# Optimization experiments

Hardware: AMD Instinct MI355X
Metric: run time of the kernel (lower is better)

## Reference

```python
import jax, jax.numpy as jnp
import numpy as np

N = 50000
E = 800000
NFEAT, NHID, NCLASS = 128, 64, 16


def _spmm(row, col, w, x):
    # out[i] = sum_{e: row[e]==i} w[e] * x[col[e]]  -- sparse adj @ x
    return jax.ops.segment_sum(x[col] * w[:, None], row, num_segments=N)


def _gcn_layer(x, row, col, w, W, b):
    return _spmm(row, col, w, x @ W) + b


def setup_inputs() -> dict:
    key = jax.random.key(0)
    ks = jax.random.split(key, 16)
    glorot = lambda k, fi, fo: jax.random.uniform(k, (fi, fo), jnp.float32, -1.0, 1.0) / jnp.sqrt(fi)
    inp = {
        "x": jax.random.normal(ks[0], (N, NFEAT), jnp.float32),
        "edge_row": jax.random.randint(ks[1], (E,), 0, N, jnp.int32),
        "edge_col": jax.random.randint(ks[2], (E,), 0, N, jnp.int32),
        "edge_weight": jax.random.uniform(ks[3], (E,), jnp.float32),
        "W1": glorot(ks[4], NFEAT, NHID), "b1": jnp.zeros((NHID,), jnp.float32),
        "W2": glorot(ks[5], NHID, NHID), "b2": jnp.zeros((NHID,), jnp.float32),
        "W3": glorot(ks[6], NHID, NHID), "b3": jnp.zeros((NHID,), jnp.float32),
        "W4": glorot(ks[7], NHID, NHID), "b4": jnp.zeros((NHID,), jnp.float32),
        "W5": glorot(ks[8], NHID, NCLASS), "b5": jnp.zeros((NCLASS,), jnp.float32),
    }
    return inp


def reference(x, edge_row, edge_col, edge_weight, W1, b1, W2, b2, W3, b3, W4, b4, W5, b5):
    # Inference mode: dropout is identity.
    e1 = _gcn_layer(x, edge_row, edge_col, edge_weight, W1, b1)
    h = jax.nn.relu(e1)
    e2 = _gcn_layer(h, edge_row, edge_col, edge_weight, W2, b2)
    h = jax.nn.relu(e2)
    e3 = _gcn_layer(h, edge_row, edge_col, edge_weight, W3, b3)
    h = jax.nn.relu(e3)
    e4 = _gcn_layer(h, edge_row, edge_col, edge_weight, W4, b4)
    h = jax.nn.relu(e4)
    e5 = _gcn_layer(h, edge_row, edge_col, edge_weight, W5, b5)
    return (jax.nn.log_softmax(e5, axis=1), e1, e2, e3, e4, e5)
```

## Files before the change

kernel.cpp:

```cpp
#include <hip/hip_runtime.h>
#include <math.h>

#define NN 50000
#define NE 800000
#define NFEAT 128
#define NHID 64
#define NCLASS 16
#define NB_SCAN ((NN + 255) / 256)
#define GB ((NN + 63) / 64)
#define SGRP 4
#define ROWS_PER_SGRP ((NN + SGRP - 1) / SGRP)
#define SCHUNKS 392
#define EMAX 1024

__device__ inline unsigned short f2bf(float f) {
    unsigned u = __builtin_bit_cast(unsigned, f);
    u += 0x7fffu + ((u >> 16) & 1u);
    return (unsigned short)(u >> 16);
}
__device__ inline float bf2f(unsigned short h) {
    return __builtin_bit_cast(float, (unsigned)h << 16);
}
__device__ inline float pk_w(unsigned v) { return bf2f((unsigned short)(v >> 16)); }
__device__ inline int pk_c(unsigned v) { return (int)(v & 0xffffu); }


__global__ __launch_bounds__(256) void hist_pack_kernel(const int* __restrict__ erow,
                                                        const int* __restrict__ ecol,
                                                        const float* __restrict__ ew,
                                                        int* __restrict__ deg,
                                                        uint2* __restrict__ rr8, int E) {
    int e = blockIdx.x * 256 + threadIdx.x;
    if (e < E) {
        int r = erow[e];
        int k = atomicAdd(&deg[r], 1);
        uint2 v;
        v.x = ((unsigned)r << 16) | (unsigned)k;
        v.y = ((unsigned)f2bf(ew[e]) << 16) | (unsigned)ecol[e];
        rr8[e] = v;
    }
}

__global__ __launch_bounds__(256) void scan_sum_kernel(const int* __restrict__ deg,
                                                       int* __restrict__ blocksum, int n) {
    __shared__ int s[256];
    const int t = threadIdx.x;
    int i = blockIdx.x * 256 + t;
    s[t] = (i < n) ? deg[i] : 0;
    __syncthreads();
#pragma unroll
    for (int off = 128; off > 0; off >>= 1) {
        if (t < off) s[t] += s[t + off];
        __syncthreads();
    }
    if (t == 0) blocksum[blockIdx.x] = s[0];
}

__global__ __launch_bounds__(256) void scan_final_kernel(const int* __restrict__ deg,
                                                         const int* __restrict__ blocksum,
                                                         int* __restrict__ row_ptr, int n) {
    __shared__ int bs[256];
    __shared__ int s[256];
    const int t = threadIdx.x;
    bs[t] = (t < NB_SCAN) ? blocksum[t] : 0;
    __syncthreads();
    for (int off = 1; off < 256; off <<= 1) {
        int u = (t >= off) ? bs[t - off] : 0;
        __syncthreads();
        bs[t] += u;
        __syncthreads();
    }
    const int blockpre = (blockIdx.x == 0) ? 0 : bs[blockIdx.x - 1];

    int i = blockIdx.x * 256 + t;
    int d = (i < n) ? deg[i] : 0;
    s[t] = d;
    __syncthreads();
    for (int off = 1; off < 256; off <<= 1) {
        int u = (t >= off) ? s[t - off] : 0;
        __syncthreads();
        s[t] += u;
        __syncthreads();
    }
    int excl = blockpre + s[t] - d;
    if (i < n) {
        row_ptr[i] = excl;
        if (i == n - 1) row_ptr[n] = excl + d;
    }
}

__global__ __launch_bounds__(256) void scatter_rank8_kernel(const uint2* __restrict__ rr8,
                                                            const int* __restrict__ row_ptr,
                                                            unsigned* __restrict__ pk, int E) {
    const int g = blockIdx.x & (SGRP - 1);
    const int chunk = blockIdx.x / SGRP;
    const int CH = (E + SCHUNKS - 1) / SCHUNKS;
    const int lo = chunk * CH;
    const int hi = (lo + CH < E) ? lo + CH : E;
    const int rlo = g * ROWS_PER_SGRP;
    const int rhi = (rlo + ROWS_PER_SGRP < NN) ? rlo + ROWS_PER_SGRP : NN;
    for (int e = lo + threadIdx.x; e < hi; e += 256) {
        uint2 v = rr8[e];
        int r = (int)(v.x >> 16);
        if (r >= rlo && r < rhi) {
            pk[row_ptr[r] + (int)(v.x & 0xffffu)] = v.y;
        }
    }
}

template <int K, bool RELU_IN>
__global__ __launch_bounds__(256) void gemm64_kernel(const float* __restrict__ in,
                                                     const float* __restrict__ Wg,
                                                     unsigned short* __restrict__ outb, int M) {
    constexpr int KC = 64;
    __shared__ float xs[KC][68];
    __shared__ float Ws[KC][64];
    const int t = threadIdx.x;
    const int tx = t % 16;
    const int ty = t / 16;
    const int r0 = blockIdx.x * 64;

    float acc[4][4];
#pragma unroll
    for (int i = 0; i < 4; i++)
#pragma unroll
        for (int j = 0; j < 4; j++) acc[i][j] = 0.f;

    for (int k0 = 0; k0 < K; k0 += KC) {
        for (int i = t * 4; i < KC * 64; i += 1024) {
            *(float4*)&Ws[i / 64][i % 64] = *(const float4*)&Wg[(size_t)k0 * 64 + i];
        }
        {
            const int r = t / 4;
            const int q = t % 4;
            const int gr = r0 + r;
#pragma unroll
            for (int i = 0; i < 4; i++) {
                int k = q * 16 + i * 4;
                float4 v;
                if (gr < M)
                    v = *(const float4*)&in[(size_t)gr * K + k0 + k];
                else
                    v = make_float4(0.f, 0.f, 0.f, 0.f);
                if (RELU_IN) {
                    v.x = fmaxf(v.x, 0.f);
                    v.y = fmaxf(v.y, 0.f);
                    v.z = fmaxf(v.z, 0.f);
                    v.w = fmaxf(v.w, 0.f);
                }
                xs[k + 0][r] = v.x;
                xs[k + 1][r] = v.y;
                xs[k + 2][r] = v.z;
                xs[k + 3][r] = v.w;
            }
        }
        __syncthreads();
#pragma unroll 8
        for (int k = 0; k < KC; k++) {
            float4 xv = *(const float4*)&xs[k][ty * 4];
            float4 wv = *(const float4*)&Ws[k][tx * 4];
            acc[0][0] += xv.x * wv.x; acc[0][1] += xv.x * wv.y;
            acc[0][2] += xv.x * wv.z; acc[0][3] += xv.x * wv.w;
            acc[1][0] += xv.y * wv.x; acc[1][1] += xv.y * wv.y;
            acc[1][2] += xv.y * wv.z; acc[1][3] += xv.y * wv.w;
            acc[2][0] += xv.z * wv.x; acc[2][1] += xv.z * wv.y;
            acc[2][2] += xv.z * wv.z; acc[2][3] += xv.z * wv.w;
            acc[3][0] += xv.w * wv.x; acc[3][1] += xv.w * wv.y;
            acc[3][2] += xv.w * wv.z; acc[3][3] += xv.w * wv.w;
        }
        __syncthreads();
    }
#pragma unroll
    for (int i = 0; i < 4; i++) {
        int r = r0 + ty * 4 + i;
        if (r < M) {
            ushort4 u;
            u.x = f2bf(acc[i][0]);
            u.y = f2bf(acc[i][1]);
            u.z = f2bf(acc[i][2]);
            u.w = f2bf(acc[i][3]);
            *(ushort4*)&outb[(size_t)r * 64 + tx * 4] = u;
        }
    }
}

template <int NOUT>
__global__ __launch_bounds__(256, 8) void spmm64_fused_kernel(
    const unsigned short* __restrict__ gb,
    const int* __restrict__ row_ptr,
    const unsigned* __restrict__ pk,
    const float* __restrict__ bias,
    const float* __restrict__ Wn,
    float* __restrict__ e_out,
    unsigned short* __restrict__ nxt,
    int M) {
    __shared__ float xs[8][64];
    __shared__ unsigned epk[EMAX];
    const int t = threadIdx.x;
    const int lane = t & 63;
    const int rb = t >> 5;
    const int slot = (lane >> 4) & 1;
    const int fl = (lane & 15) * 4;

    const int blk0 = blockIdx.x * 8;
    const int base = row_ptr[blk0];
    const int cnt = row_ptr[blk0 + 8] - base;
    const bool fits = (cnt <= EMAX);
    if (fits) {
        for (int i = t; i < cnt; i += 256) epk[i] = pk[base + i];
    }
    __syncthreads();

    const int r = blk0 + rb;
    float a0 = 0.f, a1 = 0.f, a2 = 0.f, a3 = 0.f;

#define FMA_EDGE(q, g)                                              \
    {                                                               \
        float w_ = pk_w(q);                                         \
        a0 += w_ * bf2f((unsigned short)((g).x & 0xffffu));         \
        a1 += w_ * bf2f((unsigned short)((g).x >> 16));             \
        a2 += w_ * bf2f((unsigned short)((g).y & 0xffffu));         \
        a3 += w_ * bf2f((unsigned short)((g).y >> 16));             \
    }
#define GLD(q) (*(const uint2*)&gb[(size_t)pk_c(q) * 64 + fl])

    if (fits) {
        int le = row_ptr[r] - base;
        const int lend = row_ptr[r + 1] - base;
        for (; le + 16 <= lend; le += 16) {
            unsigned q0 = epk[le + 0 + slot], q1 = epk[le + 2 + slot];
            unsigned q2 = epk[le + 4 + slot], q3 = epk[le + 6 + slot];
            unsigned q4 = epk[le + 8 + slot], q5 = epk[le + 10 + slot];
            unsigned q6 = epk[le + 12 + slot], q7 = epk[le + 14 + slot];
            uint2 g0 = GLD(q0), g1 = GLD(q1), g2 = GLD(q2), g3 = GLD(q3);
            uint2 g4 = GLD(q4), g5 = GLD(q5), g6 = GLD(q6), g7 = GLD(q7);
            FMA_EDGE(q0, g0); FMA_EDGE(q1, g1); FMA_EDGE(q2, g2); FMA_EDGE(q3, g3);
            FMA_EDGE(q4, g4); FMA_EDGE(q5, g5); FMA_EDGE(q6, g6); FMA_EDGE(q7, g7);
        }
        if (le + 8 <= lend) {
            unsigned q0 = epk[le + 0 + slot], q1 = epk[le + 2 + slot];
            unsigned q2 = epk[le + 4 + slot], q3 = epk[le + 6 + slot];
            uint2 g0 = GLD(q0), g1 = GLD(q1), g2 = GLD(q2), g3 = GLD(q3);
            FMA_EDGE(q0, g0); FMA_EDGE(q1, g1); FMA_EDGE(q2, g2); FMA_EDGE(q3, g3);
            le += 8;
        }
        if (le + 4 <= lend) {
            unsigned q0 = epk[le + 0 + slot], q1 = epk[le + 2 + slot];
            uint2 g0 = GLD(q0), g1 = GLD(q1);
            FMA_EDGE(q0, g0); FMA_EDGE(q1, g1);
            le += 4;
        }
        if (le + 2 <= lend) {
            unsigned q = epk[le + slot];
            uint2 g = GLD(q);
            FMA_EDGE(q, g);
            le += 2;
        }
        if (le < lend && slot == 0) {
            unsigned q = epk[le];
            uint2 g = GLD(q);
            FMA_EDGE(q, g);
        }
    } else {
        int e = row_ptr[r];
        const int end = row_ptr[r + 1];
        for (; e + 2 <= end; e += 2) {
            unsigned q = pk[e + slot];
            uint2 g = GLD(q);
            FMA_EDGE(q, g);
        }
        if (e < end && slot == 0) {
            unsigned q = pk[e];
            uint2 g = GLD(q);
            FMA_EDGE(q, g);
        }
    }
#undef FMA_EDGE
#undef GLD

    a0 += __shfl_xor(a0, 16);
    a1 += __shfl_xor(a1, 16);
    a2 += __shfl_xor(a2, 16);
    a3 += __shfl_xor(a3, 16);

    if (slot == 0) {
        float4 b4 = *(const float4*)&bias[fl];
        float4 v;
        v.x = a0 + b4.x;
        v.y = a1 + b4.y;
        v.z = a2 + b4.z;
        v.w = a3 + b4.w;
        *(float4*)&e_out[(size_t)r * 64 + fl] = v;
        xs[rb][fl + 0] = fmaxf(v.x, 0.f);
        xs[rb][fl + 1] = fmaxf(v.y, 0.f);
        xs[rb][fl + 2] = fmaxf(v.z, 0.f);
        xs[rb][fl + 3] = fmaxf(v.w, 0.f);
    }
    __syncthreads();

    if (NOUT == 64) {
        const int rblk = t >> 6;
        const int j = t & 63;
        float acc0 = 0.f, acc1 = 0.f;
#pragma unroll 16
        for (int k = 0; k < 64; k++) {
            float w = Wn[k * 64 + j];
            acc0 += xs[rblk][k] * w;
            acc1 += xs[rblk + 4][k] * w;
        }
        nxt[(size_t)(blk0 + rblk) * 64 + j] = f2bf(acc0);
        nxt[(size_t)(blk0 + rblk + 4) * 64 + j] = f2bf(acc1);
    } else {
        if (t < 8 * NOUT) {
            const int rr = t / NOUT;
            const int j = t % NOUT;
            float acc = 0.f;
#pragma unroll 16
            for (int k = 0; k < 64; k++) acc += xs[rr][k] * Wn[k * NOUT + j];
            nxt[(size_t)(blk0 + rr) * NOUT + j] = f2bf(acc);
        }
    }
}

__global__ __launch_bounds__(256) void spmm16_lsm_kernel(const unsigned short* __restrict__ tmpc,
                                                         const int* __restrict__ row_ptr,
                                                         const unsigned* __restrict__ pk,
                                                         const float* __restrict__ bias,
                                                         float* __restrict__ e5,
                                                         float* __restrict__ out0, int M) {
    const int t = threadIdx.x;
    const int wv = __builtin_amdgcn_readfirstlane(t >> 6);
    const int lane = t & 63;
    const int f = lane & 15;
    const int s = lane >> 4;
    const int r = blockIdx.x * 4 + wv;
    if (r >= M) return;

    int e = row_ptr[r];
    const int end = row_ptr[r + 1];
    float acc = 0.f;
    for (; e + 8 <= end; e += 8) {
        unsigned qa = pk[e + s];
        unsigned qb = pk[e + 4 + s];
        acc += pk_w(qa) * bf2f(tmpc[(size_t)pk_c(qa) * 16 + f]);
        acc += pk_w(qb) * bf2f(tmpc[(size_t)pk_c(qb) * 16 + f]);
    }
    if (e + 4 <= end) {
        unsigned q = pk[e + s];
        acc += pk_w(q) * bf2f(tmpc[(size_t)pk_c(q) * 16 + f]);
        e += 4;
    }
    if (s < end - e) {
        unsigned q = pk[e + s];
        acc += pk_w(q) * bf2f(tmpc[(size_t)pk_c(q) * 16 + f]);
    }
    acc += __shfl_xor(acc, 16);
    acc += __shfl_xor(acc, 32);
    float v = acc + bias[f];

    float m = v;
#pragma unroll
    for (int off = 1; off < 16; off <<= 1) m = fmaxf(m, __shfl_xor(m, off, 16));
    float sum = expf(v - m);
#pragma unroll
    for (int off = 1; off < 16; off <<= 1) sum += __shfl_xor(sum, off, 16);
    float ls = logf(sum);
    if (lane < 16) {
        e5[(size_t)r * 16 + f] = v;
        out0[(size_t)r * 16 + f] = v - m - ls;
    }
}


extern "C" void kernel_launch(void* const* d_in, const int* in_sizes, int n_in,
                              void* d_out, int out_size, void* d_ws, size_t ws_size,
                              hipStream_t stream) {
    const float* x = (const float*)d_in[0];
    const int* erow = (const int*)d_in[1];
    const int* ecol = (const int*)d_in[2];
    const float* ew = (const float*)d_in[3];
    const float* W1 = (const float*)d_in[4];
    const float* b1 = (const float*)d_in[5];
    const float* W2 = (const float*)d_in[6];
    const float* b2 = (const float*)d_in[7];
    const float* W3 = (const float*)d_in[8];
    const float* b3 = (const float*)d_in[9];
    const float* W4 = (const float*)d_in[10];
    const float* b4 = (const float*)d_in[11];
    const float* W5 = (const float*)d_in[12];
    const float* b5 = (const float*)d_in[13];

    float* out0 = (float*)d_out;
    float* e1 = out0 + (size_t)NN * NCLASS;
    float* e2 = e1 + (size_t)NN * NHID;
    float* e3 = e2 + (size_t)NN * NHID;
    float* e4 = e3 + (size_t)NN * NHID;
    float* e5 = e4 + (size_t)NN * NHID;

    char* ws = (char*)d_ws;
    unsigned short* tmpA = (unsigned short*)ws; ws += (size_t)NN * NHID * 2;
    unsigned short* tmpB = (unsigned short*)ws; ws += (size_t)NN * NHID * 2;
    unsigned short* tmpc = (unsigned short*)ws; ws += ((size_t)NN * NCLASS * 2 + 255) / 256 * 256;
    int* deg = (int*)ws;      ws += ((size_t)NN * 4 + 255) / 256 * 256;
    int* row_ptr = (int*)ws;  ws += ((size_t)(NN + 1) * 4 + 255) / 256 * 256;
    int* blocksum = (int*)ws; ws += ((size_t)NB_SCAN * 4 + 255) / 256 * 256;
    uint2* rr8 = (uint2*)ws;  ws += (size_t)NE * 8;
    unsigned* pk = (unsigned*)ws; ws += (size_t)NE * 4;

    hipMemsetAsync(deg, 0, (size_t)NN * 4, stream);
    hist_pack_kernel<<<(NE + 255) / 256, 256, 0, stream>>>(erow, ecol, ew, deg, rr8, NE);
    scan_sum_kernel<<<NB_SCAN, 256, 0, stream>>>(deg, blocksum, NN);
    scan_final_kernel<<<NB_SCAN, 256, 0, stream>>>(deg, blocksum, row_ptr, NN);
    scatter_rank8_kernel<<<SGRP * SCHUNKS, 256, 0, stream>>>(rr8, row_ptr, pk, NE);

    gemm64_kernel<NFEAT, false><<<GB, 256, 0, stream>>>(x, W1, tmpA, NN);

    const int FG = NN / 8;
    spmm64_fused_kernel<64><<<FG, 256, 0, stream>>>(tmpA, row_ptr, pk, b1, W2, e1, tmpB, NN);
    spmm64_fused_kernel<64><<<FG, 256, 0, stream>>>(tmpB, row_ptr, pk, b2, W3, e2, tmpA, NN);
    spmm64_fused_kernel<64><<<FG, 256, 0, stream>>>(tmpA, row_ptr, pk, b3, W4, e3, tmpB, NN);
    spmm64_fused_kernel<16><<<FG, 256, 0, stream>>>(tmpB, row_ptr, pk, b4, W5, e4, tmpc, NN);

    spmm16_lsm_kernel<<<(NN + 3) / 4, 256, 0, stream>>>(tmpc, row_ptr, pk, b5, e5, out0, NN);
}
```

Measured before the change: 306.3 us.

## Split 64-wide feature tables into two 32-column halves and run SpMM per half

The bf16 intermediate feature table is stored as two separate N×32 halves. Each 64-wide SpMM layer becomes two passes: one that gathers only the low half (about 3.2 MB, more likely to stay resident in L2/LLC) and one that gathers the high half, reloads the low result from e_out and fuses the next GEMM. The final 16-class SpMM plus log-softmax kernel is also rewritten to stage edges in shared memory and use vectorized 4-feature gathers. The trade-off is twice as many SpMM launches, edge-list reads and row_ptr work per layer, plus an extra read-back of e_out.

```diff
diff --git a/kernel.cpp b/kernel.cpp
--- a/kernel.cpp
+++ b/kernel.cpp
@@ -12,6 +12,7 @@
 #define ROWS_PER_SGRP ((NN + SGRP - 1) / SGRP)
 #define SCHUNKS 392
 #define EMAX 1024
+#define EMAX4 512
 
 __device__ inline unsigned short f2bf(float f) {
     unsigned u = __builtin_bit_cast(unsigned, f);
@@ -111,7 +112,8 @@
 template <int K, bool RELU_IN>
 __global__ __launch_bounds__(256) void gemm64_kernel(const float* __restrict__ in,
                                                      const float* __restrict__ Wg,
-                                                     unsigned short* __restrict__ outb, int M) {
+                                                     unsigned short* __restrict__ outlo,
+                                                     unsigned short* __restrict__ outhi, int M) {
     constexpr int KC = 64;
     __shared__ float xs[KC][68];
     __shared__ float Ws[KC][64];
@@ -179,28 +181,34 @@
             u.y = f2bf(acc[i][1]);
             u.z = f2bf(acc[i][2]);
             u.w = f2bf(acc[i][3]);
-            *(ushort4*)&outb[(size_t)r * 64 + tx * 4] = u;
-        }
-    }
-}
-
-template <int NOUT>
-__global__ __launch_bounds__(256, 8) void spmm64_fused_kernel(
-    const unsigned short* __restrict__ gb,
-    const int* __restrict__ row_ptr,
-    const unsigned* __restrict__ pk,
-    const float* __restrict__ bias,
-    const float* __restrict__ Wn,
-    float* __restrict__ e_out,
-    unsigned short* __restrict__ nxt,
-    int M) {
-    __shared__ float xs[8][64];
+            if (tx < 8)
+                *(ushort4*)&outlo[(size_t)r * 32 + tx * 4] = u;
+            else
+                *(ushort4*)&outhi[(size_t)r * 32 + tx * 4 - 32] = u;
+        }
+    }
+}
+
+#define FMA_EDGE(q, g)                                      \
+    {                                                       \
+        float w_ = pk_w(q);                                 \
+        a0 += w_ * bf2f((unsigned short)((g).x & 0xffffu)); \
+        a1 += w_ * bf2f((unsigned short)((g).x >> 16));     \
+        a2 += w_ * bf2f((unsigned short)((g).y & 0xffffu)); \
+        a3 += w_ * bf2f((unsigned short)((g).y >> 16));     \
+    }
+#define GLD32(tbl, q) (*(const uint2*)&(tbl)[(size_t)pk_c(q) * 32 + fl])
+
+__global__ __launch_bounds__(256, 8) void spmm_lo_kernel(
+    const unsigned short* __restrict__ tlo, const int* __restrict__ row_ptr,
+    const unsigned* __restrict__ pk, const float* __restrict__ bias,
+    float* __restrict__ e_out, int M) {
     __shared__ unsigned epk[EMAX];
     const int t = threadIdx.x;
     const int lane = t & 63;
     const int rb = t >> 5;
-    const int slot = (lane >> 4) & 1;
-    const int fl = (lane & 15) * 4;
+    const int sl = (lane >> 3) & 3;
+    const int fl = (lane & 7) * 4;
 
     const int blk0 = blockIdx.x * 8;
     const int base = row_ptr[blk0];
@@ -213,88 +221,164 @@
 
     const int r = blk0 + rb;
     float a0 = 0.f, a1 = 0.f, a2 = 0.f, a3 = 0.f;
-
-#define FMA_EDGE(q, g)                                              \
-    {                                                               \
-        float w_ = pk_w(q);                                         \
-        a0 += w_ * bf2f((unsigned short)((g).x & 0xffffu));         \
-        a1 += w_ * bf2f((unsigned short)((g).x >> 16));             \
-        a2 += w_ * bf2f((unsigned short)((g).y & 0xffffu));         \
-        a3 += w_ * bf2f((unsigned short)((g).y >> 16));             \
-    }
-#define GLD(q) (*(const uint2*)&gb[(size_t)pk_c(q) * 64 + fl])
-
     if (fits) {
         int le = row_ptr[r] - base;
         const int lend = row_ptr[r + 1] - base;
-        for (; le + 16 <= lend; le += 16) {
-            unsigned q0 = epk[le + 0 + slot], q1 = epk[le + 2 + slot];
-            unsigned q2 = epk[le + 4 + slot], q3 = epk[le + 6 + slot];
-            unsigned q4 = epk[le + 8 + slot], q5 = epk[le + 10 + slot];
-            unsigned q6 = epk[le + 12 + slot], q7 = epk[le + 14 + slot];
-            uint2 g0 = GLD(q0), g1 = GLD(q1), g2 = GLD(q2), g3 = GLD(q3);
-            uint2 g4 = GLD(q4), g5 = GLD(q5), g6 = GLD(q6), g7 = GLD(q7);
+        for (; le + 32 <= lend; le += 32) {
+            unsigned q0 = epk[le + 0 + sl], q1 = epk[le + 4 + sl], q2 = epk[le + 8 + sl],
+                     q3 = epk[le + 12 + sl], q4 = epk[le + 16 + sl], q5 = epk[le + 20 + sl],
+                     q6 = epk[le + 24 + sl], q7 = epk[le + 28 + sl];
+            uint2 g0 = GLD32(tlo, q0), g1 = GLD32(tlo, q1), g2 = GLD32(tlo, q2), g3 = GLD32(tlo, q3);
+            uint2 g4 = GLD32(tlo, q4), g5 = GLD32(tlo, q5), g6 = GLD32(tlo, q6), g7 = GLD32(tlo, q7);
             FMA_EDGE(q0, g0); FMA_EDGE(q1, g1); FMA_EDGE(q2, g2); FMA_EDGE(q3, g3);
             FMA_EDGE(q4, g4); FMA_EDGE(q5, g5); FMA_EDGE(q6, g6); FMA_EDGE(q7, g7);
         }
+        if (le + 16 <= lend) {
+            unsigned q0 = epk[le + sl], q1 = epk[le + 4 + sl], q2 = epk[le + 8 + sl],
+                     q3 = epk[le + 12 + sl];
+            uint2 g0 = GLD32(tlo, q0), g1 = GLD32(tlo, q1), g2 = GLD32(tlo, q2), g3 = GLD32(tlo, q3);
+            FMA_EDGE(q0, g0); FMA_EDGE(q1, g1); FMA_EDGE(q2, g2); FMA_EDGE(q3, g3);
+            le += 16;
+        }
         if (le + 8 <= lend) {
-            unsigned q0 = epk[le + 0 + slot], q1 = epk[le + 2 + slot];
-            unsigned q2 = epk[le + 4 + slot], q3 = epk[le + 6 + slot];
-            uint2 g0 = GLD(q0), g1 = GLD(q1), g2 = GLD(q2), g3 = GLD(q3);
-            FMA_EDGE(q0, g0); FMA_EDGE(q1, g1); FMA_EDGE(q2, g2); FMA_EDGE(q3, g3);
+            unsigned q0 = epk[le + sl], q1 = epk[le + 4 + sl];
+            uint2 g0 = GLD32(tlo, q0), g1 = GLD32(tlo, q1);
+            FMA_EDGE(q0, g0); FMA_EDGE(q1, g1);
             le += 8;
         }
         if (le + 4 <= lend) {
-            unsigned q0 = epk[le + 0 + slot], q1 = epk[le + 2 + slot];
-            uint2 g0 = GLD(q0), g1 = GLD(q1);
-            FMA_EDGE(q0, g0); FMA_EDGE(q1, g1);
+            unsigned q = epk[le + sl];
+            uint2 g = GLD32(tlo, q);
+            FMA_EDGE(q, g);
             le += 4;
         }
-        if (le + 2 <= lend) {
-            unsigned q = epk[le + slot];
-            uint2 g = GLD(q);
-            FMA_EDGE(q, g);
-            le += 2;
-        }
-        if (le < lend && slot == 0) {
-            unsigned q = epk[le];
-            uint2 g = GLD(q);
+        int rem = lend - le;
+        if (sl < rem) {
+            unsigned q = epk[le + sl];
+            uint2 g = GLD32(tlo, q);
             FMA_EDGE(q, g);
         }
     } else {
         int e = row_ptr[r];
-        const int end = row_ptr[r + 1];
-        for (; e + 2 <= end; e += 2) {
-            unsigned q = pk[e + slot];
-            uint2 g = GLD(q);
-            FMA_EDGE(q, g);
-        }
-        if (e < end && slot == 0) {
-            unsigned q = pk[e];
-            uint2 g = GLD(q);
-            FMA_EDGE(q, g);
-        }
-    }
-#undef FMA_EDGE
-#undef GLD
-
-    a0 += __shfl_xor(a0, 16);
-    a1 += __shfl_xor(a1, 16);
-    a2 += __shfl_xor(a2, 16);
-    a3 += __shfl_xor(a3, 16);
-
-    if (slot == 0) {
+        const int e1 = row_ptr[r + 1];
+        for (; e + 4 <= e1; e += 4) {
+            unsigned q = pk[e + sl];
+            uint2 g = GLD32(tlo, q);
+            FMA_EDGE(q, g);
+        }
+        int rem = e1 - e;
+        if (sl < rem) {
+            unsigned q = pk[e + sl];
+            uint2 g = GLD32(tlo, q);
+            FMA_EDGE(q, g);
+        }
+    }
+    a0 += __shfl_xor(a0, 8); a0 += __shfl_xor(a0, 16);
+    a1 += __shfl_xor(a1, 8); a1 += __shfl_xor(a1, 16);
+    a2 += __shfl_xor(a2, 8); a2 += __shfl_xor(a2, 16);
+    a3 += __shfl_xor(a3, 8); a3 += __shfl_xor(a3, 16);
+    if (sl == 0) {
         float4 b4 = *(const float4*)&bias[fl];
         float4 v;
-        v.x = a0 + b4.x;
-        v.y = a1 + b4.y;
-        v.z = a2 + b4.z;
-        v.w = a3 + b4.w;
+        v.x = a0 + b4.x; v.y = a1 + b4.y; v.z = a2 + b4.z; v.w = a3 + b4.w;
         *(float4*)&e_out[(size_t)r * 64 + fl] = v;
-        xs[rb][fl + 0] = fmaxf(v.x, 0.f);
-        xs[rb][fl + 1] = fmaxf(v.y, 0.f);
-        xs[rb][fl + 2] = fmaxf(v.z, 0.f);
-        xs[rb][fl + 3] = fmaxf(v.w, 0.f);
+    }
+}
+
+template <int NOUT>
+__global__ __launch_bounds__(256, 8) void spmm_hi_kernel(
+    const unsigned short* __restrict__ thi, const int* __restrict__ row_ptr,
+    const unsigned* __restrict__ pk, const float* __restrict__ bias,
+    const float* __restrict__ Wn, float* __restrict__ e_out,
+    unsigned short* __restrict__ nlo, unsigned short* __restrict__ nhi, int M) {
+    __shared__ unsigned epk[EMAX];
+    __shared__ float xs[8][64];
+    const int t = threadIdx.x;
+    const int lane = t & 63;
+    const int rb = t >> 5;
+    const int sl = (lane >> 3) & 3;
+    const int fl = (lane & 7) * 4;
+
+    const int blk0 = blockIdx.x * 8;
+    float elo = e_out[(size_t)(blk0 + (t >> 5)) * 64 + (t & 31)];
+
+    const int base = row_ptr[blk0];
+    const int cnt = row_ptr[blk0 + 8] - base;
+    const bool fits = (cnt <= EMAX);
+    if (fits) {
+        for (int i = t; i < cnt; i += 256) epk[i] = pk[base + i];
+    }
+    __syncthreads();
+
+    const int r = blk0 + rb;
+    float a0 = 0.f, a1 = 0.f, a2 = 0.f, a3 = 0.f;
+    if (fits) {
+        int le = row_ptr[r] - base;
+        const int lend = row_ptr[r + 1] - base;
+        for (; le + 32 <= lend; le += 32) {
+            unsigned q0 = epk[le + 0 + sl], q1 = epk[le + 4 + sl], q2 = epk[le + 8 + sl],
+                     q3 = epk[le + 12 + sl], q4 = epk[le + 16 + sl], q5 = epk[le + 20 + sl],
+                     q6 = epk[le + 24 + sl], q7 = epk[le + 28 + sl];
+            uint2 g0 = GLD32(thi, q0), g1 = GLD32(thi, q1), g2 = GLD32(thi, q2), g3 = GLD32(thi, q3);
+            uint2 g4 = GLD32(thi, q4), g5 = GLD32(thi, q5), g6 = GLD32(thi, q6), g7 = GLD32(thi, q7);
+            FMA_EDGE(q0, g0); FMA_EDGE(q1, g1); FMA_EDGE(q2, g2); FMA_EDGE(q3, g3);
+            FMA_EDGE(q4, g4); FMA_EDGE(q5, g5); FMA_EDGE(q6, g6); FMA_EDGE(q7, g7);
+        }
+        if (le + 16 <= lend) {
+            unsigned q0 = epk[le + sl], q1 = epk[le + 4 + sl], q2 = epk[le + 8 + sl],
+                     q3 = epk[le + 12 + sl];
+            uint2 g0 = GLD32(thi, q0), g1 = GLD32(thi, q1), g2 = GLD32(thi, q2), g3 = GLD32(thi, q3);
+            FMA_EDGE(q0, g0); FMA_EDGE(q1, g1); FMA_EDGE(q2, g2); FMA_EDGE(q3, g3);
+            le += 16;
+        }
+        if (le + 8 <= lend) {
+            unsigned q0 = epk[le + sl], q1 = epk[le + 4 + sl];
+            uint2 g0 = GLD32(thi, q0), g1 = GLD32(thi, q1);
+            FMA_EDGE(q0, g0); FMA_EDGE(q1, g1);
+            le += 8;
+        }
+        if (le + 4 <= lend) {
+            unsigned q = epk[le + sl];
+            uint2 g = GLD32(thi, q);
+            FMA_EDGE(q, g);
+            le += 4;
+        }
+        int rem = lend - le;
+        if (sl < rem) {
+            unsigned q = epk[le + sl];
+            uint2 g = GLD32(thi, q);
+            FMA_EDGE(q, g);
+        }
+    } else {
+        int e = row_ptr[r];
+        const int e1 = row_ptr[r + 1];
+        for (; e + 4 <= e1; e += 4) {
+            unsigned q = pk[e + sl];
+            uint2 g = GLD32(thi, q);
+            FMA_EDGE(q, g);
+        }
+        int rem = e1 - e;
+        if (sl < rem) {
+            unsigned q = pk[e + sl];
+            uint2 g = GLD32(thi, q);
+            FMA_EDGE(q, g);
+        }
+    }
+    a0 += __shfl_xor(a0, 8); a0 += __shfl_xor(a0, 16);
+    a1 += __shfl_xor(a1, 8); a1 += __shfl_xor(a1, 16);
+    a2 += __shfl_xor(a2, 8); a2 += __shfl_xor(a2, 16);
+    a3 += __shfl_xor(a3, 8); a3 += __shfl_xor(a3, 16);
+
+    xs[t >> 5][t & 31] = fmaxf(elo, 0.f);
+    if (sl == 0) {
+        float4 b4 = *(const float4*)&bias[32 + fl];
+        float4 v;
+        v.x = a0 + b4.x; v.y = a1 + b4.y; v.z = a2 + b4.z; v.w = a3 + b4.w;
+        *(float4*)&e_out[(size_t)r * 64 + 32 + fl] = v;
+        xs[rb][32 + fl + 0] = fmaxf(v.x, 0.f);
+        xs[rb][32 + fl + 1] = fmaxf(v.y, 0.f);
+        xs[rb][32 + fl + 2] = fmaxf(v.z, 0.f);
+        xs[rb][32 + fl + 3] = fmaxf(v.w, 0.f);
     }
     __syncthreads();
 
@@ -308,8 +392,13 @@
             acc0 += xs[rblk][k] * w;
             acc1 += xs[rblk + 4][k] * w;
         }
-        nxt[(size_t)(blk0 + rblk) * 64 + j] = f2bf(acc0);
-        nxt[(size_t)(blk0 + rblk + 4) * 64 + j] = f2bf(acc1);
+        if (j < 32) {
+            nlo[(size_t)(blk0 + rblk) * 32 + j] = f2bf(acc0);
+            nlo[(size_t)(blk0 + rblk + 4) * 32 + j] = f2bf(acc1);
+        } else {
+            nhi[(size_t)(blk0 + rblk) * 32 + j - 32] = f2bf(acc0);
+            nhi[(size_t)(blk0 + rblk + 4) * 32 + j - 32] = f2bf(acc1);
+        }
     } else {
         if (t < 8 * NOUT) {
             const int rr = t / NOUT;
@@ -317,57 +406,88 @@
             float acc = 0.f;
 #pragma unroll 16
             for (int k = 0; k < 64; k++) acc += xs[rr][k] * Wn[k * NOUT + j];
-            nxt[(size_t)(blk0 + rr) * NOUT + j] = f2bf(acc);
-        }
-    }
-}
-
-__global__ __launch_bounds__(256) void spmm16_lsm_kernel(const unsigned short* __restrict__ tmpc,
-                                                         const int* __restrict__ row_ptr,
-                                                         const unsigned* __restrict__ pk,
-                                                         const float* __restrict__ bias,
-                                                         float* __restrict__ e5,
-                                                         float* __restrict__ out0, int M) {
+            nlo[(size_t)(blk0 + rr) * NOUT + j] = f2bf(acc);
+        }
+    }
+}
+
+__global__ __launch_bounds__(256, 8) void spmm16_lsm_kernel(const unsigned short* __restrict__ tmpc,
+                                                            const int* __restrict__ row_ptr,
+                                                            const unsigned* __restrict__ pk,
+                                                            const float* __restrict__ bias,
+                                                            float* __restrict__ e5,
+                                                            float* __restrict__ out0, int M) {
+    __shared__ unsigned epk[EMAX4];
     const int t = threadIdx.x;
-    const int wv = __builtin_amdgcn_readfirstlane(t >> 6);
     const int lane = t & 63;
-    const int f = lane & 15;
-    const int s = lane >> 4;
-    const int r = blockIdx.x * 4 + wv;
-    if (r >= M) return;
-
-    int e = row_ptr[r];
-    const int end = row_ptr[r + 1];
-    float acc = 0.f;
-    for (; e + 8 <= end; e += 8) {
-        unsigned qa = pk[e + s];
-        unsigned qb = pk[e + 4 + s];
-        acc += pk_w(qa) * bf2f(tmpc[(size_t)pk_c(qa) * 16 + f]);
-        acc += pk_w(qb) * bf2f(tmpc[(size_t)pk_c(qb) * 16 + f]);
-    }
-    if (e + 4 <= end) {
-        unsigned q = pk[e + s];
-        acc += pk_w(q) * bf2f(tmpc[(size_t)pk_c(q) * 16 + f]);
-        e += 4;
-    }
-    if (s < end - e) {
-        unsigned q = pk[e + s];
-        acc += pk_w(q) * bf2f(tmpc[(size_t)pk_c(q) * 16 + f]);
-    }
-    acc += __shfl_xor(acc, 16);
-    acc += __shfl_xor(acc, 32);
-    float v = acc + bias[f];
-
-    float m = v;
+    const int wv = t >> 6;
+    const int sl = lane >> 2;
+    const int fq = (lane & 3) * 4;
+
+    const int blk0 = blockIdx.x * 4;
+    const int base = row_ptr[blk0];
+    const int cnt = row_ptr[blk0 + 4] - base;
+    const bool fits = (cnt <= EMAX4);
+    if (fits) {
+        for (int i = t; i < cnt; i += 256) epk[i] = pk[base + i];
+    }
+    __syncthreads();
+
+    const int r = blk0 + wv;
+    float a0 = 0.f, a1 = 0.f, a2 = 0.f, a3 = 0.f;
+#define GLD16(q) (*(const uint2*)&tmpc[(size_t)pk_c(q) * 16 + fq])
+    if (fits) {
+        int le = row_ptr[r] - base;
+        const int lend = row_ptr[r + 1] - base;
+        for (; le + 16 <= lend; le += 16) {
+            unsigned q = epk[le + sl];
+            uint2 g = GLD16(q);
+            FMA_EDGE(q, g);
+        }
+        int rem = lend - le;
+        if (sl < rem) {
+            unsigned q = epk[le + sl];
+            uint2 g = GLD16(q);
+            FMA_EDGE(q, g);
+        }
+    } else {
+        int e = row_ptr[r];
+        const int e1 = row_ptr[r + 1];
+        for (; e + 16 <= e1; e += 16) {
+            unsigned q = pk[e + sl];
+            uint2 g = GLD16(q);
+            FMA_EDGE(q, g);
+        }
+        int rem = e1 - e;
+        if (sl < rem) {
+            unsigned q = pk[e + sl];
+            uint2 g = GLD16(q);
+            FMA_EDGE(q, g);
+        }
+    }
+#undef GLD16
 #pragma unroll
-    for (int off = 1; off < 16; off <<= 1) m = fmaxf(m, __shfl_xor(m, off, 16));
-    float sum = expf(v - m);
-#pragma unroll
-    for (int off = 1; off < 16; off <<= 1) sum += __shfl_xor(sum, off, 16);
-    float ls = logf(sum);
-    if (lane < 16) {
-        e5[(size_t)r * 16 + f] = v;
-        out0[(size_t)r * 16 + f] = v - m - ls;
+    for (int off = 4; off < 64; off <<= 1) {
+        a0 += __shfl_xor(a0, off);
+        a1 += __shfl_xor(a1, off);
+        a2 += __shfl_xor(a2, off);
+        a3 += __shfl_xor(a3, off);
+    }
+    float4 b4 = *(const float4*)&bias[fq];
+    float v0 = a0 + b4.x, v1 = a1 + b4.y, v2 = a2 + b4.z, v3 = a3 + b4.w;
+
+    float m = fmaxf(fmaxf(v0, v1), fmaxf(v2, v3));
+    m = fmaxf(m, __shfl_xor(m, 1));
+    m = fmaxf(m, __shfl_xor(m, 2));
+    float s = expf(v0 - m) + expf(v1 - m) + expf(v2 - m) + expf(v3 - m);
+    s += __shfl_xor(s, 1);
+    s += __shfl_xor(s, 2);
+    float ls = logf(s) + m;
+    if (lane < 4) {
+        float4 ev = make_float4(v0, v1, v2, v3);
+        *(float4*)&e5[(size_t)r * 16 + fq] = ev;
+        float4 ov = make_float4(v0 - ls, v1 - ls, v2 - ls, v3 - ls);
+        *(float4*)&out0[(size_t)r * 16 + fq] = ov;
     }
 }
 
@@ -398,8 +518,10 @@
     float* e5 = e4 + (size_t)NN * NHID;
 
     char* ws = (char*)d_ws;
-    unsigned short* tmpA = (unsigned short*)ws; ws += (size_t)NN * NHID * 2;
-    unsigned short* tmpB = (unsigned short*)ws; ws += (size_t)NN * NHID * 2;
+    unsigned short* tAlo = (unsigned short*)ws; ws += (size_t)NN * 32 * 2;
+    unsigned short* tAhi = (unsigned short*)ws; ws += (size_t)NN * 32 * 2;
+    unsigned short* tBlo = (unsigned short*)ws; ws += (size_t)NN * 32 * 2;
+    unsigned short* tBhi = (unsigned short*)ws; ws += (size_t)NN * 32 * 2;
     unsigned short* tmpc = (unsigned short*)ws; ws += ((size_t)NN * NCLASS * 2 + 255) / 256 * 256;
     int* deg = (int*)ws;      ws += ((size_t)NN * 4 + 255) / 256 * 256;
     int* row_ptr = (int*)ws;  ws += ((size_t)(NN + 1) * 4 + 255) / 256 * 256;
@@ -413,13 +535,17 @@
     scan_final_kernel<<<NB_SCAN, 256, 0, stream>>>(deg, blocksum, row_ptr, NN);
     scatter_rank8_kernel<<<SGRP * SCHUNKS, 256, 0, stream>>>(rr8, row_ptr, pk, NE);
 
-    gemm64_kernel<NFEAT, false><<<GB, 256, 0, stream>>>(x, W1, tmpA, NN);
+    gemm64_kernel<NFEAT, false><<<GB, 256, 0, stream>>>(x, W1, tAlo, tAhi, NN);
 
     const int FG = NN / 8;
-    spmm64_fused_kernel<64><<<FG, 256, 0, stream>>>(tmpA, row_ptr, pk, b1, W2, e1, tmpB, NN);
-    spmm64_fused_kernel<64><<<FG, 256, 0, stream>>>(tmpB, row_ptr, pk, b2, W3, e2, tmpA, NN);
-    spmm64_fused_kernel<64><<<FG, 256, 0, stream>>>(tmpA, row_ptr, pk, b3, W4, e3, tmpB, NN);
-    spmm64_fused_kernel<16><<<FG, 256, 0, stream>>>(tmpB, row_ptr, pk, b4, W5, e4, tmpc, NN);
+    spmm_lo_kernel<<<FG, 256, 0, stream>>>(tAlo, row_ptr, pk, b1, e1, NN);
+    spmm_hi_kernel<64><<<FG, 256, 0, stream>>>(tAhi, row_ptr, pk, b1, W2, e1, tBlo, tBhi, NN);
+    spmm_lo_kernel<<<FG, 256, 0, stream>>>(tBlo, row_ptr, pk, b2, e2, NN);
+    spmm_hi_kernel<64><<<FG, 256, 0, stream>>>(tBhi, row_ptr, pk, b2, W3, e2, tAlo, tAhi, NN);
+    spmm_lo_kernel<<<FG, 256, 0, stream>>>(tAlo, row_ptr, pk, b3, e3, NN);
+    spmm_hi_kernel<64><<<FG, 256, 0, stream>>>(tAhi, row_ptr, pk, b3, W4, e3, tBlo, tBhi, NN);
+    spmm_lo_kernel<<<FG, 256, 0, stream>>>(tBlo, row_ptr, pk, b4, e4, NN);
+    spmm_hi_kernel<16><<<FG, 256, 0, stream>>>(tBhi, row_ptr, pk, b4, W5, e4, tmpc, nullptr, NN);
 
     spmm16_lsm_kernel<<<(NN + 3) / 4, 256, 0, stream>>>(tmpc, row_ptr, pk, b5, e5, out0, NN);
 }
```

Result: slower. 353.8 us (+15.5%).
